# Kernel tuning notes

Measured on AMD Instinct MI355X. Metric: run time of the kernel, lower is better.

The kernel has to match this reference:

```python
import jax, jax.numpy as jnp
import numpy as np

NUM_HEADS = 16

def _rms_norm(x):
    # F.rms_norm over last dim, eps = dtype machine epsilon (torch default eps=None)
    eps = jnp.finfo(jnp.float32).eps
    ms = jnp.mean(jnp.square(x.astype(jnp.float32)), axis=-1, keepdims=True)
    return (x.astype(jnp.float32) * jax.lax.rsqrt(ms + eps)).astype(x.dtype)

def _rotary_tables(T, head_dim):
    # inv_freq = (1/1024)**linspace(0,1,head_dim//4), padded with zeros to head_dim//2
    quarter = head_dim // 4
    inv_freq = (1.0 / 1024.0) ** jnp.linspace(0.0, 1.0, quarter, dtype=jnp.float32)
    inv_freq = jnp.concatenate([inv_freq, jnp.zeros(quarter, dtype=jnp.float32)])
    t = jnp.arange(T, dtype=jnp.float32)
    theta = t[:, None] * inv_freq[None, :]          # [T, head_dim//2]
    return jnp.cos(theta), jnp.sin(theta)

def _rotary(x, cos, sin):
    # x: [B, T, H, hd]; rotate in fp32, cast back
    xf = x.astype(jnp.float32)
    x1, x2 = jnp.split(xf, 2, axis=-1)
    c = cos[None, :, None, :]
    s = sin[None, :, None, :]
    y1 = x1 * c + x2 * s
    y2 = -x1 * s + x2 * c
    return jnp.concatenate([y1, y2], axis=-1).astype(x.dtype)

def setup_inputs() -> dict:
    key = jax.random.key(0)
    ks = jax.random.split(key, 7)
    B, T, D = 1, 2048, 1024
    sc = 1.0 / np.sqrt(D)
    return {
        "x": jax.random.normal(ks[0], (B, T, D), jnp.float32),
        "vi": jax.random.normal(ks[1], (B, T, D), jnp.float32),
        "Wq": jax.random.normal(ks[2], (D, D), jnp.float32) * sc,
        "Wk": jax.random.normal(ks[3], (D, D), jnp.float32) * sc,
        "Wv": jax.random.normal(ks[4], (D, D), jnp.float32) * sc,
        "Wproj": jax.random.normal(ks[5], (D, D), jnp.float32) * sc,
        "lambdas": jnp.array([0.5, 0.5], jnp.float32),
    }

def reference(x, vi, Wq, Wk, Wv, Wproj, lambdas):
    B, T, D = x.shape
    H = NUM_HEADS
    hd = D // H
    q = (x @ Wq.T).reshape(B, T, H, hd)
    k = (x @ Wk.T).reshape(B, T, H, hd)
    v = (x @ Wv.T).reshape(B, T, H, hd)
    # value residual: lambda-mixed v
    v = lambdas[0] * v + lambdas[1] * vi.reshape(B, T, H, hd)
    q, k = _rms_norm(q), _rms_norm(k)
    cos, sin = _rotary_tables(T, hd)
    q, k = _rotary(q, cos, sin), _rotary(k, cos, sin)
    # causal attention, default flex_attention scale = 1/sqrt(head_dim)
    scores = jnp.einsum('bthd,bshd->bhts', q, k) / jnp.sqrt(jnp.float32(hd))
    causal = jnp.tril(jnp.ones((T, T), dtype=bool))
    scores = jnp.where(causal[None, None], scores, jnp.float32(-1e30))
    attn = jax.nn.softmax(scores, axis=-1)
    y = jnp.einsum('bhts,bshd->bthd', attn, v).reshape(B, T, D)
    return y @ Wproj.T
```

## Files before the change

kernel.cpp:

```cpp
#include <hip/hip_runtime.h>
#include <math.h>

#define T_SEQ 2048
#define D_MODEL 1024
#define NH 16
#define HD 64

typedef unsigned short ushort_t;
typedef unsigned int uint_t;
typedef short short8 __attribute__((ext_vector_type(8)));
typedef float floatx4 __attribute__((ext_vector_type(4)));

__device__ __forceinline__ ushort_t f2bf(float f) {
    uint_t u = __float_as_uint(f);
    u += 0x7FFFu + ((u >> 16) & 1u);
    return (ushort_t)(u >> 16);
}
__device__ __forceinline__ uint_t pack2(float a, float b) {
    return (uint_t)f2bf(a) | ((uint_t)f2bf(b) << 16);
}
__device__ __forceinline__ void cp16(ushort_t* dst, const ushort_t* src) {
    uint4 a = ((const uint4*)src)[0];
    uint4 b = ((const uint4*)src)[1];
    ((uint4*)dst)[0] = a;
    ((uint4*)dst)[1] = b;
}

#define LDB 72
#define LDK 72

__global__ __launch_bounds__(256) void to_bf16(
        const float* __restrict__ x,  const float* __restrict__ wq,
        const float* __restrict__ wk, const float* __restrict__ wv,
        const float* __restrict__ wp,
        ushort_t* __restrict__ xb,  ushort_t* __restrict__ wqb,
        ushort_t* __restrict__ wkb, ushort_t* __restrict__ wvb,
        ushort_t* __restrict__ wpb)
{
    size_t i = (size_t)blockIdx.x * 256 + threadIdx.x;
    const float* src; ushort_t* dst; size_t off;
    if (i < 262144)      { src = x;  dst = xb;  off = i; }
    else if (i < 393216) { src = wq; dst = wqb; off = i - 262144; }
    else if (i < 524288) { src = wk; dst = wkb; off = i - 393216; }
    else if (i < 655360) { src = wv; dst = wvb; off = i - 524288; }
    else                 { src = wp; dst = wpb; off = i - 655360; }
    float4 f0 = ((const float4*)src)[off * 2];
    float4 f1 = ((const float4*)src)[off * 2 + 1];
    uint4 u;
    u.x = pack2(f0.x, f0.y); u.y = pack2(f0.z, f0.w);
    u.z = pack2(f1.x, f1.y); u.w = pack2(f1.z, f1.w);
    ((uint4*)dst)[off] = u;
}

__global__ __launch_bounds__(256) void gemm_qkv(
        const ushort_t* __restrict__ xb,
        const ushort_t* __restrict__ Wqb, const ushort_t* __restrict__ Wkb,
        const ushort_t* __restrict__ Wvb,
        const float* __restrict__ vi, const float* __restrict__ lam,
        ushort_t* __restrict__ qb, ushort_t* __restrict__ kb,
        ushort_t* __restrict__ vbt)
{
    const int z = blockIdx.z;
    const ushort_t* __restrict__ W = (z == 0) ? Wqb : (z == 1) ? Wkb : Wvb;
    const int row0 = blockIdx.y * 128;
    const int col0 = blockIdx.x * 128;

    __shared__ ushort_t As[128 * LDB];
    __shared__ ushort_t Bs[128 * LDB];

    const int tid = threadIdx.x;
    const int wave = tid >> 6, lane = tid & 63;
    const int wm = wave >> 1, wn = wave & 1;
    const int l15 = lane & 15, quad = lane >> 4;
    const int r_st = tid >> 1;
    const int c_st = (tid & 1) * 32;

    floatx4 acc[4][4];
    #pragma unroll
    for (int i = 0; i < 4; ++i)
        #pragma unroll
        for (int j = 0; j < 4; ++j)
            acc[i][j] = (floatx4){0.f, 0.f, 0.f, 0.f};

    for (int k0 = 0; k0 < D_MODEL; k0 += 64) {
        __syncthreads();
        cp16(As + r_st * LDB + c_st,      xb + (size_t)(row0 + r_st) * D_MODEL + k0 + c_st);
        cp16(As + r_st * LDB + c_st + 16, xb + (size_t)(row0 + r_st) * D_MODEL + k0 + c_st + 16);
        cp16(Bs + r_st * LDB + c_st,      W  + (size_t)(col0 + r_st) * D_MODEL + k0 + c_st);
        cp16(Bs + r_st * LDB + c_st + 16, W  + (size_t)(col0 + r_st) * D_MODEL + k0 + c_st + 16);
        __syncthreads();
        #pragma unroll
        for (int kh = 0; kh < 2; ++kh) {
            short8 a[4], b[4];
            #pragma unroll
            for (int i = 0; i < 4; ++i) {
                a[i] = *(const short8*)(As + (64 * wm + i * 16 + l15) * LDB + kh * 32 + quad * 8);
                b[i] = *(const short8*)(Bs + (64 * wn + i * 16 + l15) * LDB + kh * 32 + quad * 8);
            }
            #pragma unroll
            for (int i = 0; i < 4; ++i)
                #pragma unroll
                for (int j = 0; j < 4; ++j)
                    acc[i][j] = __builtin_amdgcn_mfma_f32_16x16x32_bf16(a[i], b[j], acc[i][j], 0, 0, 0);
        }
    }

    if (z < 2) {
        ushort_t* __restrict__ o = (z == 0) ? qb : kb;
        const float oscale = (z == 0) ? 0.125f : 1.0f;
        const int hbase = col0 + 64 * wn;
        const float eps = 1.1920929e-7f;
        const float fr = exp2f(-10.0f * (float)l15 / 15.0f);
        #pragma unroll
        for (int i = 0; i < 4; ++i)
            #pragma unroll
            for (int r = 0; r < 4; ++r) {
                const int t = row0 + 64 * wm + i * 16 + quad * 4 + r;
                float v0 = acc[i][0][r], v1 = acc[i][1][r];
                float v2 = acc[i][2][r], v3 = acc[i][3][r];
                float ss = v0 * v0 + v1 * v1 + v2 * v2 + v3 * v3;
                ss += __shfl_xor(ss, 1);
                ss += __shfl_xor(ss, 2);
                ss += __shfl_xor(ss, 4);
                ss += __shfl_xor(ss, 8);
                const float sc = rsqrtf(ss * (1.0f / 64.0f) + eps);
                v0 *= sc; v1 *= sc; v2 *= sc; v3 *= sc;
                const float th = (float)t * fr;
                const float cs = cosf(th), sn = sinf(th);
                const float y0 = v0 * cs + v2 * sn;
                const float y2 = v2 * cs - v0 * sn;
                const size_t rb = (size_t)t * D_MODEL + hbase;
                o[rb +  0 + l15] = f2bf(y0 * oscale);
                o[rb + 16 + l15] = f2bf(v1 * oscale);
                o[rb + 32 + l15] = f2bf(y2 * oscale);
                o[rb + 48 + l15] = f2bf(v3 * oscale);
            }
    } else {
        const float l0 = lam[0], l1 = lam[1];
        #pragma unroll
        for (int i = 0; i < 4; ++i)
            #pragma unroll
            for (int j = 0; j < 4; ++j) {
                const int tb = row0 + 64 * wm + i * 16 + quad * 4;
                const int jj = col0 + 64 * wn + j * 16 + l15;
                float b0 = l0 * acc[i][j][0] + l1 * vi[(size_t)(tb + 0) * D_MODEL + jj];
                float b1 = l0 * acc[i][j][1] + l1 * vi[(size_t)(tb + 1) * D_MODEL + jj];
                float b2 = l0 * acc[i][j][2] + l1 * vi[(size_t)(tb + 2) * D_MODEL + jj];
                float b3 = l0 * acc[i][j][3] + l1 * vi[(size_t)(tb + 3) * D_MODEL + jj];
                uint2 u;
                u.x = pack2(b0, b1);
                u.y = pack2(b2, b3);
                *(uint2*)(vbt + (size_t)jj * T_SEQ + tb) = u;
            }
    }
}

__global__ __launch_bounds__(256) void attn(
        const ushort_t* __restrict__ qb, const ushort_t* __restrict__ kb,
        const ushort_t* __restrict__ vbt, ushort_t* __restrict__ yb,
        float* __restrict__ Opart, float* __restrict__ Lpart)
{
    const int h = blockIdx.y;
    const int x = blockIdx.x;
    int qt, ct_begin, ct_end, pidx;
    if (x < 16) {
        qt = 31 - x;
        const int mid = (qt + 2) >> 1;
        ct_begin = 0; ct_end = mid;
        pidx = ((h * 16 + (qt - 16)) << 1);
    } else if (x < 32) {
        qt = 47 - x;
        const int mid = (qt + 2) >> 1;
        ct_begin = mid; ct_end = qt + 1;
        pidx = ((h * 16 + (qt - 16)) << 1) + 1;
    } else {
        qt = 47 - x;
        ct_begin = 0; ct_end = qt + 1;
        pidx = -1;
    }
    const int t0 = qt * 64;

    __shared__ ushort_t Ks[64 * LDK];
    __shared__ ushort_t Vs[64 * LDK];
    __shared__ ushort_t QPs[64 * LDK];

    const int tid = threadIdx.x;
    const int wave = tid >> 6, lane = tid & 63;
    const int l15 = lane & 15, quad = lane >> 4;
    const int r4 = tid >> 2, c4 = (tid & 3) * 16;

    cp16(QPs + r4 * LDK + c4, qb + (size_t)(t0 + r4) * D_MODEL + h * HD + c4);
    __syncthreads();
    short8 qf[2];
    qf[0] = *(const short8*)(QPs + (16 * wave + l15) * LDK + 0  + quad * 8);
    qf[1] = *(const short8*)(QPs + (16 * wave + l15) * LDK + 32 + quad * 8);

    float l_acc[4];
    floatx4 O[4];
    #pragma unroll
    for (int r = 0; r < 4; ++r) l_acc[r] = 0.0f;
    #pragma unroll
    for (int d = 0; d < 4; ++d) O[d] = (floatx4){0.f, 0.f, 0.f, 0.f};

    for (int kt = ct_begin; kt < ct_end; ++kt) {
        const int s0 = kt * 64;
        __syncthreads();
        cp16(Ks + r4 * LDK + c4, kb  + (size_t)(s0 + r4) * D_MODEL + h * HD + c4);
        cp16(Vs + r4 * LDK + c4, vbt + (size_t)(h * HD + r4) * T_SEQ + s0 + c4);
        __syncthreads();

        floatx4 sa[4];
        #pragma unroll
        for (int ct = 0; ct < 4; ++ct) {
            short8 b0 = *(const short8*)(Ks + (ct * 16 + l15) * LDK + 0  + quad * 8);
            short8 b1 = *(const short8*)(Ks + (ct * 16 + l15) * LDK + 32 + quad * 8);
            floatx4 t4 = (floatx4){0.f, 0.f, 0.f, 0.f};
            t4 = __builtin_amdgcn_mfma_f32_16x16x32_bf16(qf[0], b0, t4, 0, 0, 0);
            t4 = __builtin_amdgcn_mfma_f32_16x16x32_bf16(qf[1], b1, t4, 0, 0, 0);
            sa[ct] = t4;
        }
        if (kt == qt) {
            #pragma unroll
            for (int ct = 0; ct < 4; ++ct)
                #pragma unroll
                for (int r = 0; r < 4; ++r) {
                    int trow = 16 * wave + quad * 4 + r;
                    int scol = ct * 16 + l15;
                    if (scol > trow) sa[ct][r] = -1e30f;
                }
        }
        float p[4][4];
        #pragma unroll
        for (int ct = 0; ct < 4; ++ct)
            #pragma unroll
            for (int r = 0; r < 4; ++r) {
                p[ct][r] = __expf(sa[ct][r] - 8.0f);
                l_acc[r] += p[ct][r];
            }

        #pragma unroll
        for (int ct = 0; ct < 4; ++ct)
            #pragma unroll
            for (int r = 0; r < 4; ++r)
                QPs[(16 * wave + quad * 4 + r) * LDK + ct * 16 + l15] = f2bf(p[ct][r]);

        short8 pa0 = *(const short8*)(QPs + (16 * wave + l15) * LDK + 0  + quad * 8);
        short8 pa1 = *(const short8*)(QPs + (16 * wave + l15) * LDK + 32 + quad * 8);
        #pragma unroll
        for (int dt = 0; dt < 4; ++dt) {
            short8 vb0 = *(const short8*)(Vs + (dt * 16 + l15) * LDK + 0  + quad * 8);
            short8 vb1 = *(const short8*)(Vs + (dt * 16 + l15) * LDK + 32 + quad * 8);
            O[dt] = __builtin_amdgcn_mfma_f32_16x16x32_bf16(pa0, vb0, O[dt], 0, 0, 0);
            O[dt] = __builtin_amdgcn_mfma_f32_16x16x32_bf16(pa1, vb1, O[dt], 0, 0, 0);
        }
    }

    float l_run[4];
    #pragma unroll
    for (int r = 0; r < 4; ++r) {
        float s = l_acc[r];
        s += __shfl_xor(s, 1);
        s += __shfl_xor(s, 2);
        s += __shfl_xor(s, 4);
        s += __shfl_xor(s, 8);
        l_run[r] = s;
    }

    if (pidx < 0) {
        #pragma unroll
        for (int r = 0; r < 4; ++r) {
            const float inv_l = 1.0f / l_run[r];
            const int t = t0 + 16 * wave + quad * 4 + r;
            #pragma unroll
            for (int dt = 0; dt < 4; ++dt)
                yb[(size_t)t * D_MODEL + h * HD + dt * 16 + l15] = f2bf(O[dt][r] * inv_l);
        }
    } else {
        float* __restrict__ Op = Opart + (size_t)pidx * 4096;
        #pragma unroll
        for (int r = 0; r < 4; ++r) {
            const int row = 16 * wave + quad * 4 + r;
            #pragma unroll
            for (int dt = 0; dt < 4; ++dt)
                Op[row * 64 + dt * 16 + l15] = O[dt][r];
            if (l15 == 0) Lpart[(size_t)pidx * 64 + row] = l_run[r];
        }
    }
}

__global__ __launch_bounds__(256) void attn_combine(
        const float* __restrict__ Opart, const float* __restrict__ Lpart,
        ushort_t* __restrict__ yb)
{
    const int qtp = blockIdx.x;
    const int h   = blockIdx.y;
    const int tid = threadIdx.x;
    const int row  = tid >> 2;
    const int dseg = (tid & 3) * 16;
    const int p0 = (h * 16 + qtp) * 2;

    const float l0 = Lpart[(size_t)p0 * 64 + row];
    const float l1 = Lpart[((size_t)p0 + 1) * 64 + row];
    const float inv = 1.0f / (l0 + l1);

    const float* O0 = Opart + (size_t)p0 * 4096 + row * 64 + dseg;
    const float* O1 = O0 + 4096;

    uint_t u[8];
    #pragma unroll
    for (int g = 0; g < 4; ++g) {
        float4 a = ((const float4*)O0)[g];
        float4 b = ((const float4*)O1)[g];
        u[g * 2 + 0] = pack2((a.x + b.x) * inv, (a.y + b.y) * inv);
        u[g * 2 + 1] = pack2((a.z + b.z) * inv, (a.w + b.w) * inv);
    }
    const int t = (16 + qtp) * 64 + row;
    uint4* dst = (uint4*)(yb + (size_t)t * D_MODEL + h * HD + dseg);
    dst[0] = make_uint4(u[0], u[1], u[2], u[3]);
    dst[1] = make_uint4(u[4], u[5], u[6], u[7]);
}

__global__ __launch_bounds__(256) void gemm_proj(
        const ushort_t* __restrict__ yb, const ushort_t* __restrict__ Wpb,
        float* __restrict__ out)
{
    const int row0 = blockIdx.y * 128;
    const int col0 = blockIdx.x * 128;

    __shared__ ushort_t As[128 * LDB];
    __shared__ ushort_t Bs[128 * LDB];

    const int tid = threadIdx.x;
    const int wave = tid >> 6, lane = tid & 63;
    const int wm = wave >> 1, wn = wave & 1;
    const int l15 = lane & 15, quad = lane >> 4;
    const int r_st = tid >> 1;
    const int c_st = (tid & 1) * 32;

    floatx4 acc[4][4];
    #pragma unroll
    for (int i = 0; i < 4; ++i)
        #pragma unroll
        for (int j = 0; j < 4; ++j)
            acc[i][j] = (floatx4){0.f, 0.f, 0.f, 0.f};

    for (int k0 = 0; k0 < D_MODEL; k0 += 64) {
        __syncthreads();
        cp16(As + r_st * LDB + c_st,      yb  + (size_t)(row0 + r_st) * D_MODEL + k0 + c_st);
        cp16(As + r_st * LDB + c_st + 16, yb  + (size_t)(row0 + r_st) * D_MODEL + k0 + c_st + 16);
        cp16(Bs + r_st * LDB + c_st,      Wpb + (size_t)(col0 + r_st) * D_MODEL + k0 + c_st);
        cp16(Bs + r_st * LDB + c_st + 16, Wpb + (size_t)(col0 + r_st) * D_MODEL + k0 + c_st + 16);
        __syncthreads();
        #pragma unroll
        for (int kh = 0; kh < 2; ++kh) {
            short8 a[4], b[4];
            #pragma unroll
            for (int i = 0; i < 4; ++i) {
                a[i] = *(const short8*)(As + (64 * wm + i * 16 + l15) * LDB + kh * 32 + quad * 8);
                b[i] = *(const short8*)(Bs + (64 * wn + i * 16 + l15) * LDB + kh * 32 + quad * 8);
            }
            #pragma unroll
            for (int i = 0; i < 4; ++i)
                #pragma unroll
                for (int j = 0; j < 4; ++j)
                    acc[i][j] = __builtin_amdgcn_mfma_f32_16x16x32_bf16(a[i], b[j], acc[i][j], 0, 0, 0);
        }
    }

    #pragma unroll
    for (int i = 0; i < 4; ++i)
        #pragma unroll
        for (int j = 0; j < 4; ++j) {
            const int t = row0 + 64 * wm + i * 16 + quad * 4;
            const int jj = col0 + 64 * wn + j * 16 + l15;
            #pragma unroll
            for (int r = 0; r < 4; ++r)
                out[(size_t)(t + r) * D_MODEL + jj] = acc[i][j][r];
        }
}

extern "C" void kernel_launch(void* const* d_in, const int* in_sizes, int n_in,
                              void* d_out, int out_size, void* d_ws, size_t ws_size,
                              hipStream_t stream) {
    (void)in_sizes; (void)n_in; (void)out_size; (void)ws_size;
    const float* x   = (const float*)d_in[0];
    const float* vi  = (const float*)d_in[1];
    const float* Wq  = (const float*)d_in[2];
    const float* Wk  = (const float*)d_in[3];
    const float* Wv  = (const float*)d_in[4];
    const float* Wp  = (const float*)d_in[5];
    const float* lam = (const float*)d_in[6];

    char* base = (char*)d_ws;
    ushort_t* xb  = (ushort_t*)(base);
    ushort_t* wqb = (ushort_t*)(base + (size_t)4  * 1048576);
    ushort_t* wkb = (ushort_t*)(base + (size_t)6  * 1048576);
    ushort_t* wvb = (ushort_t*)(base + (size_t)8  * 1048576);
    ushort_t* wpb = (ushort_t*)(base + (size_t)10 * 1048576);
    ushort_t* qb  = (ushort_t*)(base + (size_t)12 * 1048576);
    ushort_t* kb  = (ushort_t*)(base + (size_t)16 * 1048576);
    ushort_t* vbt = (ushort_t*)(base + (size_t)20 * 1048576);
    ushort_t* yb  = (ushort_t*)(base + (size_t)24 * 1048576);
    float* Opart  = (float*)(base);
    float* Lpart  = (float*)(base + (size_t)8 * 1048576);
    float* out = (float*)d_out;

    to_bf16<<<dim3(786432 / 256), 256, 0, stream>>>(x, Wq, Wk, Wv, Wp, xb, wqb, wkb, wvb, wpb);
    gemm_qkv<<<dim3(8, 16, 3), 256, 0, stream>>>(xb, wqb, wkb, wvb, vi, lam, qb, kb, vbt);
    attn<<<dim3(48, 16), 256, 0, stream>>>(qb, kb, vbt, yb, Opart, Lpart);
    attn_combine<<<dim3(16, 16), 256, 0, stream>>>(Opart, Lpart, yb);
    gemm_proj<<<dim3(8, 16), 256, 0, stream>>>(yb, wpb, out);
}
```

Baseline: 170.7 us.

## Use direct global-to-LDS loads with XOR swizzle and 64-row tiles in GEMMs

```diff
diff --git a/kernel.cpp b/kernel.cpp
--- a/kernel.cpp
+++ b/kernel.cpp
@@ -25,8 +25,12 @@
     ((uint4*)dst)[0] = a;
     ((uint4*)dst)[1] = b;
 }
-
-#define LDB 72
+__device__ __forceinline__ void gload16(const ushort_t* g, ushort_t* l) {
+    __builtin_amdgcn_global_load_lds(
+        (const __attribute__((address_space(1))) void*)g,
+        (__attribute__((address_space(3))) void*)l, 16, 0, 0);
+}
+
 #define LDK 72
 
 __global__ __launch_bounds__(256) void to_bf16(
@@ -62,43 +66,49 @@
 {
     const int z = blockIdx.z;
     const ushort_t* __restrict__ W = (z == 0) ? Wqb : (z == 1) ? Wkb : Wvb;
-    const int row0 = blockIdx.y * 128;
+    const int row0 = blockIdx.y * 64;
     const int col0 = blockIdx.x * 128;
 
-    __shared__ ushort_t As[128 * LDB];
-    __shared__ ushort_t Bs[128 * LDB];
+    __shared__ ushort_t As[64 * 64];
+    __shared__ ushort_t Bs[128 * 64];
 
     const int tid = threadIdx.x;
     const int wave = tid >> 6, lane = tid & 63;
     const int wm = wave >> 1, wn = wave & 1;
     const int l15 = lane & 15, quad = lane >> 4;
-    const int r_st = tid >> 1;
-    const int c_st = (tid & 1) * 32;
-
-    floatx4 acc[4][4];
-    #pragma unroll
-    for (int i = 0; i < 4; ++i)
+    const int srow  = tid >> 3;
+    const int sslot = (tid & 7) ^ (srow & 7);
+
+    floatx4 acc[2][4];
+    #pragma unroll
+    for (int i = 0; i < 2; ++i)
         #pragma unroll
         for (int j = 0; j < 4; ++j)
             acc[i][j] = (floatx4){0.f, 0.f, 0.f, 0.f};
 
     for (int k0 = 0; k0 < D_MODEL; k0 += 64) {
         __syncthreads();
-        cp16(As + r_st * LDB + c_st,      xb + (size_t)(row0 + r_st) * D_MODEL + k0 + c_st);
-        cp16(As + r_st * LDB + c_st + 16, xb + (size_t)(row0 + r_st) * D_MODEL + k0 + c_st + 16);
-        cp16(Bs + r_st * LDB + c_st,      W  + (size_t)(col0 + r_st) * D_MODEL + k0 + c_st);
-        cp16(Bs + r_st * LDB + c_st + 16, W  + (size_t)(col0 + r_st) * D_MODEL + k0 + c_st + 16);
+        #pragma unroll
+        for (int c = 0; c < 2; ++c)
+            gload16(xb + (size_t)(row0 + c * 32 + srow) * D_MODEL + k0 + sslot * 8,
+                    As + c * 2048 + tid * 8);
+        #pragma unroll
+        for (int c = 0; c < 4; ++c)
+            gload16(W + (size_t)(col0 + c * 32 + srow) * D_MODEL + k0 + sslot * 8,
+                    Bs + c * 2048 + tid * 8);
         __syncthreads();
         #pragma unroll
         for (int kh = 0; kh < 2; ++kh) {
-            short8 a[4], b[4];
-            #pragma unroll
-            for (int i = 0; i < 4; ++i) {
-                a[i] = *(const short8*)(As + (64 * wm + i * 16 + l15) * LDB + kh * 32 + quad * 8);
-                b[i] = *(const short8*)(Bs + (64 * wn + i * 16 + l15) * LDB + kh * 32 + quad * 8);
-            }
-            #pragma unroll
-            for (int i = 0; i < 4; ++i)
+            const int slot = ((kh * 4 + quad) ^ (l15 & 7)) << 3;
+            short8 a[2], b[4];
+            #pragma unroll
+            for (int i = 0; i < 2; ++i)
+                a[i] = *(const short8*)(As + (32 * wm + i * 16 + l15) * 64 + slot);
+            #pragma unroll
+            for (int j = 0; j < 4; ++j)
+                b[j] = *(const short8*)(Bs + (64 * wn + j * 16 + l15) * 64 + slot);
+            #pragma unroll
+            for (int i = 0; i < 2; ++i)
                 #pragma unroll
                 for (int j = 0; j < 4; ++j)
                     acc[i][j] = __builtin_amdgcn_mfma_f32_16x16x32_bf16(a[i], b[j], acc[i][j], 0, 0, 0);
@@ -112,10 +122,10 @@
         const float eps = 1.1920929e-7f;
         const float fr = exp2f(-10.0f * (float)l15 / 15.0f);
         #pragma unroll
-        for (int i = 0; i < 4; ++i)
+        for (int i = 0; i < 2; ++i)
             #pragma unroll
             for (int r = 0; r < 4; ++r) {
-                const int t = row0 + 64 * wm + i * 16 + quad * 4 + r;
+                const int t = row0 + 32 * wm + i * 16 + quad * 4 + r;
                 float v0 = acc[i][0][r], v1 = acc[i][1][r];
                 float v2 = acc[i][2][r], v3 = acc[i][3][r];
                 float ss = v0 * v0 + v1 * v1 + v2 * v2 + v3 * v3;
@@ -138,10 +148,10 @@
     } else {
         const float l0 = lam[0], l1 = lam[1];
         #pragma unroll
-        for (int i = 0; i < 4; ++i)
+        for (int i = 0; i < 2; ++i)
             #pragma unroll
             for (int j = 0; j < 4; ++j) {
-                const int tb = row0 + 64 * wm + i * 16 + quad * 4;
+                const int tb = row0 + 32 * wm + i * 16 + quad * 4;
                 const int jj = col0 + 64 * wn + j * 16 + l15;
                 float b0 = l0 * acc[i][j][0] + l1 * vi[(size_t)(tb + 0) * D_MODEL + jj];
                 float b1 = l0 * acc[i][j][1] + l1 * vi[(size_t)(tb + 1) * D_MODEL + jj];
@@ -324,43 +334,49 @@
         const ushort_t* __restrict__ yb, const ushort_t* __restrict__ Wpb,
         float* __restrict__ out)
 {
-    const int row0 = blockIdx.y * 128;
+    const int row0 = blockIdx.y * 64;
     const int col0 = blockIdx.x * 128;
 
-    __shared__ ushort_t As[128 * LDB];
-    __shared__ ushort_t Bs[128 * LDB];
+    __shared__ ushort_t As[64 * 64];
+    __shared__ ushort_t Bs[128 * 64];
 
     const int tid = threadIdx.x;
     const int wave = tid >> 6, lane = tid & 63;
     const int wm = wave >> 1, wn = wave & 1;
     const int l15 = lane & 15, quad = lane >> 4;
-    const int r_st = tid >> 1;
-    const int c_st = (tid & 1) * 32;
-
-    floatx4 acc[4][4];
-    #pragma unroll
-    for (int i = 0; i < 4; ++i)
+    const int srow  = tid >> 3;
+    const int sslot = (tid & 7) ^ (srow & 7);
+
+    floatx4 acc[2][4];
+    #pragma unroll
+    for (int i = 0; i < 2; ++i)
         #pragma unroll
         for (int j = 0; j < 4; ++j)
             acc[i][j] = (floatx4){0.f, 0.f, 0.f, 0.f};
 
     for (int k0 = 0; k0 < D_MODEL; k0 += 64) {
         __syncthreads();
-        cp16(As + r_st * LDB + c_st,      yb  + (size_t)(row0 + r_st) * D_MODEL + k0 + c_st);
-        cp16(As + r_st * LDB + c_st + 16, yb  + (size_t)(row0 + r_st) * D_MODEL + k0 + c_st + 16);
-        cp16(Bs + r_st * LDB + c_st,      Wpb + (size_t)(col0 + r_st) * D_MODEL + k0 + c_st);
-        cp16(Bs + r_st * LDB + c_st + 16, Wpb + (size_t)(col0 + r_st) * D_MODEL + k0 + c_st + 16);
+        #pragma unroll
+        for (int c = 0; c < 2; ++c)
+            gload16(yb + (size_t)(row0 + c * 32 + srow) * D_MODEL + k0 + sslot * 8,
+                    As + c * 2048 + tid * 8);
+        #pragma unroll
+        for (int c = 0; c < 4; ++c)
+            gload16(Wpb + (size_t)(col0 + c * 32 + srow) * D_MODEL + k0 + sslot * 8,
+                    Bs + c * 2048 + tid * 8);
         __syncthreads();
         #pragma unroll
         for (int kh = 0; kh < 2; ++kh) {
-            short8 a[4], b[4];
-            #pragma unroll
-            for (int i = 0; i < 4; ++i) {
-                a[i] = *(const short8*)(As + (64 * wm + i * 16 + l15) * LDB + kh * 32 + quad * 8);
-                b[i] = *(const short8*)(Bs + (64 * wn + i * 16 + l15) * LDB + kh * 32 + quad * 8);
-            }
-            #pragma unroll
-            for (int i = 0; i < 4; ++i)
+            const int slot = ((kh * 4 + quad) ^ (l15 & 7)) << 3;
+            short8 a[2], b[4];
+            #pragma unroll
+            for (int i = 0; i < 2; ++i)
+                a[i] = *(const short8*)(As + (32 * wm + i * 16 + l15) * 64 + slot);
+            #pragma unroll
+            for (int j = 0; j < 4; ++j)
+                b[j] = *(const short8*)(Bs + (64 * wn + j * 16 + l15) * 64 + slot);
+            #pragma unroll
+            for (int i = 0; i < 2; ++i)
                 #pragma unroll
                 for (int j = 0; j < 4; ++j)
                     acc[i][j] = __builtin_amdgcn_mfma_f32_16x16x32_bf16(a[i], b[j], acc[i][j], 0, 0, 0);
@@ -368,10 +384,10 @@
     }
 
     #pragma unroll
-    for (int i = 0; i < 4; ++i)
+    for (int i = 0; i < 2; ++i)
         #pragma unroll
         for (int j = 0; j < 4; ++j) {
-            const int t = row0 + 64 * wm + i * 16 + quad * 4;
+            const int t = row0 + 32 * wm + i * 16 + quad * 4;
             const int jj = col0 + 64 * wn + j * 16 + l15;
             #pragma unroll
             for (int r = 0; r < 4; ++r)
@@ -406,8 +422,8 @@
     float* out = (float*)d_out;
 
     to_bf16<<<dim3(786432 / 256), 256, 0, stream>>>(x, Wq, Wk, Wv, Wp, xb, wqb, wkb, wvb, wpb);
-    gemm_qkv<<<dim3(8, 16, 3), 256, 0, stream>>>(xb, wqb, wkb, wvb, vi, lam, qb, kb, vbt);
+    gemm_qkv<<<dim3(8, 32, 3), 256, 0, stream>>>(xb, wqb, wkb, wvb, vi, lam, qb, kb, vbt);
     attn<<<dim3(48, 16), 256, 0, stream>>>(qb, kb, vbt, yb, Opart, Lpart);
     attn_combine<<<dim3(16, 16), 256, 0, stream>>>(Opart, Lpart, yb);
-    gemm_proj<<<dim3(8, 16), 256, 0, stream>>>(yb, wpb, out);
-}
+    gemm_proj<<<dim3(8, 32), 256, 0, stream>>>(yb, wpb, out);
+}
```

After: 157.5 us. 1.08x faster.
